# Performance work log

Measured on AMD Instinct MI355X. Metric: run time of the kernel, lower is better.

Reference implementation:

```python
import jax, jax.numpy as jnp
import numpy as np
from jax import lax

RHO = 1.0
L = 50

def _pbc_index(rho=RHO, L=L):
    # S = {(m,n) | |mn| <= rho*L//2, |m|<=L//2, |n|<=L//2}; rho*L//2 == 25.0 here
    thr = (rho * L) // 2
    idx = [(m, n)
           for m in range(-L // 2, L // 2 + 1)
           for n in range(-L // 2, L // 2 + 1)
           if abs(m * n) <= thr]
    return np.asarray(idx, dtype=np.int32)  # [T, 2], T = 449


def setup_inputs() -> dict:
    key = jax.random.key(0)
    k1, k2, k3, k4 = jax.random.split(key, 4)
    B, S, Nmodes = 8, 16384, 2
    T = _pbc_index().shape[0]  # 449
    return {
        "E_real": jax.random.normal(k1, (B, S, Nmodes), dtype=jnp.float32),
        "E_imag": jax.random.normal(k2, (B, S, Nmodes), dtype=jnp.float32),
        "C_real": jax.random.normal(k3, (4, T), dtype=jnp.float32) * 0.01,
        "C_imag": jax.random.normal(k4, (4, T), dtype=jnp.float32) * 0.01,
    }


def reference(E_real, E_imag, C_real, C_imag):
    idx = _pbc_index()
    m = jnp.asarray(idx[:, 0])
    n = jnp.asarray(idx[:, 1])
    E = E_real + 1j * E_imag                 # [B, S, 2] complex64
    C = (C_real + 1j * C_imag)[0]            # task_info=None -> row 0, [T]

    # O_k,i = E_k,i + sum_{m,n} (E_{k+n,i} E*_{k+m+n,i} + E_{k+n,-i} E*_{k+m+n,-i}) E_{k+m,i} C_{m,n}
    def body(acc, term):
        mi, ni, ci = term
        A = jnp.roll(E, ni, axis=-2) * jnp.conj(jnp.roll(E, mi + ni, axis=-2))
        A = A + jnp.roll(A, 1, axis=-1)      # cross-polarization term (Nmodes=2)
        return acc + A * jnp.roll(E, mi, axis=-2) * ci, None

    acc, _ = lax.scan(body, jnp.zeros_like(E), (m, n, C))
    Eo = E + acc                             # P = 1 (task_info=None), sqrt(P)**3 = 1
    return Eo[..., L:-L, :]                  # drop overlaps: [B, S-2L, 2]
```

## Files before the change

### kernel.cpp

```cpp
#include <hip/hip_runtime.h>


typedef float v2f __attribute__((ext_vector_type(2)));
typedef float v4f __attribute__((ext_vector_type(4)));

#define S_LEN 16384
#define SOUT  16284
#define BLK   512
#define NOUT  256
#define NE    356
#define NE2   178
#define ND    307
#define ND_AL 308
#define NDP   154

constexpr int LIMS[26] = {25,25,12,8,6,5,4,3,3,2,2,2,2,
                          1,1,1,1,1,1,1,1,1,1,1,1,1};
constexpr int TS[51] = {
      0,  3,  6,  9, 12, 15, 18, 21, 24, 27, 30, 33, 36,
     39, 44, 49, 54, 59, 66, 73, 82, 93,106,123,148,199,
    250,301,326,343,356,367,376,383,390,395,400,405,410,
    413,416,419,422,425,428,431,434,437,440,443,446};

template<int M>
__device__ __forceinline__ void convM(
    const float2* __restrict__ sDm, const v4f* __restrict__ sEp,
    int o0, const float* __restrict__ Cr0, const float* __restrict__ Ci0,
    float4& acc)
{
    constexpr int lim = LIMS[M];
    constexpr int tp  = TS[25 + M];
    constexpr int tn  = TS[25 - M];
    constexpr int A   = 25 + lim;

    v2f SxP0 = {0.f,0.f}, SyP0 = {0.f,0.f}, SxP1 = {0.f,0.f}, SyP1 = {0.f,0.f};
    v2f SxN0 = {0.f,0.f}, SyN0 = {0.f,0.f}, SxN1 = {0.f,0.f}, SyN1 = {0.f,0.f};

#define TAP(dconst, dd)                                                     \
    {                                                                       \
        const int d_ = (dconst);                                            \
        if (A - d_ >= 0 && A - d_ <= 2*lim) {                               \
            const float cx = Cr0[tp + A - d_], cy = Ci0[tp + A - d_];       \
            SxP0 += cx * (dd);  SyP0 += cy * (dd);                          \
        }                                                                   \
        if (A + 1 - d_ >= 0 && A + 1 - d_ <= 2*lim) {                       \
            const float cx = Cr0[tp + A+1-d_], cy = Ci0[tp + A+1-d_];       \
            SxP1 += cx * (dd);  SyP1 += cy * (dd);                          \
        }                                                                   \
        if (A + M - d_ >= 0 && A + M - d_ <= 2*lim) {                       \
            const float cx = Cr0[tn + A+M-d_], cy = Ci0[tn + A+M-d_];       \
            SxN0 += cx * (dd);  SyN0 += cy * (dd);                          \
        }                                                                   \
        if (A + M + 1 - d_ >= 0 && A + M + 1 - d_ <= 2*lim) {               \
            const float cx = Cr0[tn + A+M+1-d_], cy = Ci0[tn + A+M+1-d_];   \
            SxN1 += cx * (dd);  SyN1 += cy * (dd);                          \
        }                                                                   \
    }

    if constexpr (M < 2*lim + 4) {
        constexpr int dlo = (25 - lim) & ~1;
        constexpr int dhi = 26 + lim + M;
        constexpr int NP  = (dhi - dlo) / 2 + 1;
        #pragma unroll
        for (int p = 0; p < NP; ++p) {
            const int d0 = dlo + 2*p;
            v4f w = *reinterpret_cast<const v4f*>(&sDm[o0 + d0]);
            TAP(d0,     w.xy)
            TAP(d0 + 1, w.zw)
        }
    } else {
        {
            constexpr int dlo = (25 - lim) & ~1;
            constexpr int dhi = 26 + lim;
            constexpr int NP  = (dhi - dlo) / 2 + 1;
            #pragma unroll
            for (int p = 0; p < NP; ++p) {
                const int d0 = dlo + 2*p;
                v4f w = *reinterpret_cast<const v4f*>(&sDm[o0 + d0]);
                #pragma unroll
                for (int e = 0; e < 2; ++e) {
                    const int d = d0 + e;
                    const v2f dd = e ? w.zw : w.xy;
                    if (A - d >= 0 && A - d <= 2*lim) {
                        const float cx = Cr0[tp + A - d], cy = Ci0[tp + A - d];
                        SxP0 += cx * dd;  SyP0 += cy * dd;
                    }
                    if (A + 1 - d >= 0 && A + 1 - d <= 2*lim) {
                        const float cx = Cr0[tp + A+1-d], cy = Ci0[tp + A+1-d];
                        SxP1 += cx * dd;  SyP1 += cy * dd;
                    }
                }
            }
        }
        {
            constexpr int dlo = (25 + M - lim) & ~1;
            constexpr int dhi = 26 + M + lim;
            constexpr int NP  = (dhi - dlo) / 2 + 1;
            #pragma unroll
            for (int p = 0; p < NP; ++p) {
                const int d0 = dlo + 2*p;
                v4f w = *reinterpret_cast<const v4f*>(&sDm[o0 + d0]);
                #pragma unroll
                for (int e = 0; e < 2; ++e) {
                    const int d = d0 + e;
                    const v2f dd = e ? w.zw : w.xy;
                    if (A + M - d >= 0 && A + M - d <= 2*lim) {
                        const float cx = Cr0[tn + A+M-d], cy = Ci0[tn + A+M-d];
                        SxN0 += cx * dd;  SyN0 += cy * dd;
                    }
                    if (A + M + 1 - d >= 0 && A + M + 1 - d <= 2*lim) {
                        const float cx = Cr0[tn + A+M+1-d], cy = Ci0[tn + A+M+1-d];
                        SxN1 += cx * dd;  SyN1 += cy * dd;
                    }
                }
            }
        }
    }
#undef TAP

    const float s0pr = SxP0.x - SyP0.y, s0pi = SxP0.y + SyP0.x;
    const float s1pr = SxP1.x - SyP1.y, s1pi = SxP1.y + SyP1.x;
    const float s0nr = SxN0.x + SyN0.y, s0ni = SyN0.x - SxN0.y;
    const float s1nr = SxN1.x + SyN1.y, s1ni = SyN1.x - SxN1.y;

    const int t = o0 >> 1;
    v4f ep0, ep1, en0, en1;
    if constexpr ((M & 1) == 0) {
        ep0 = sEp[t + (50 - M)/2];
        ep1 = sEp[t + (50 - M)/2 + NE2];
        en0 = sEp[t + (50 + M)/2];
        en1 = sEp[t + (50 + M)/2 + NE2];
    } else {
        ep0 = sEp[t + (49 - M)/2 + NE2];
        ep1 = sEp[t + (51 - M)/2];
        en0 = sEp[t + (49 + M)/2 + NE2];
        en1 = sEp[t + (51 + M)/2];
    }
    acc.x += s0pr*ep0.x - s0pi*ep0.y + s0nr*en0.x - s0ni*en0.y;
    acc.y += s0pr*ep0.z - s0pi*ep0.w + s0nr*en0.z - s0ni*en0.w;
    acc.z += s1pr*ep1.x - s1pi*ep1.y + s1nr*en1.x - s1ni*en1.y;
    acc.w += s1pr*ep1.z - s1pi*ep1.w + s1nr*en1.z - s1ni*en1.w;
}

__device__ __forceinline__ void conv0(
    const float* __restrict__ sD0p, const v4f* __restrict__ sEp,
    int o0, const float* __restrict__ Cr0, const float* __restrict__ Ci0,
    float4& acc)
{
    v2f s0 = {0.f, 0.f}, s1 = {0.f, 0.f};
    #pragma unroll
    for (int p = 0; p < 26; ++p) {
        const int d0 = 2*p;
        float2 w = *reinterpret_cast<const float2*>(&sD0p[o0 + d0]);
        #pragma unroll
        for (int e = 0; e < 2; ++e) {
            const int d = d0 + e;
            const float dv = e ? w.y : w.x;
            if (50 - d >= 0) {
                v2f cv = { Cr0[199 + 50 - d], Ci0[199 + 50 - d] };
                s0 += dv * cv;
            }
            if (51 - d <= 50 && 51 - d >= 0) {
                v2f cv = { Cr0[199 + 51 - d], Ci0[199 + 51 - d] };
                s1 += dv * cv;
            }
        }
    }
    const int t = o0 >> 1;
    v4f e0 = sEp[t + 25];
    v4f e1 = sEp[t + 25 + NE2];
    acc.x += s0.x*e0.x - s0.y*e0.y;
    acc.y += s0.x*e0.z - s0.y*e0.w;
    acc.z += s1.x*e1.x - s1.y*e1.y;
    acc.w += s1.x*e1.z - s1.y*e1.w;
}

__global__ __launch_bounds__(BLK, 4) void pbc_kernel(
    const float* __restrict__ Er, const float* __restrict__ Ei,
    const float* __restrict__ Cr, const float* __restrict__ Ci,
    float* __restrict__ out)
{
    __shared__ __align__(16) v4f    sEp[NE];
    __shared__ __align__(16) float2 sD[25][ND_AL];
    __shared__ __align__(16) float  sD0[ND_AL];
    __shared__ __align__(16) float4 sAcc[4][128];

    const int b   = blockIdx.y;
    const int k0  = blockIdx.x * NOUT;
    const int tid = threadIdx.x;

    const float* erb = Er + (size_t)b * (S_LEN * 2);
    const float* eib = Ei + (size_t)b * (S_LEN * 2);
    if (tid < NE2) {
        const int i  = tid;
        const int kg = k0 + 2 * i;
        v4f rr = {0.f,0.f,0.f,0.f}, ii = {0.f,0.f,0.f,0.f};
        if (kg < S_LEN) {
            rr = *reinterpret_cast<const v4f*>(erb + 2 * kg);
            ii = *reinterpret_cast<const v4f*>(eib + 2 * kg);
        }
        sEp[i]       = (v4f){rr.x, ii.x, rr.y, ii.y};
        sEp[i + NE2] = (v4f){rr.z, ii.z, rr.w, ii.w};
    }
    __syncthreads();

    if (tid < NDP) {
        const int xp = tid;
        v4f a0 = sEp[xp + 12 + NE2];
        v4f a1 = sEp[xp + 13];
        float d0 = a0.x*a0.x + a0.y*a0.y + a0.z*a0.z + a0.w*a0.w;
        float d1 = a1.x*a1.x + a1.y*a1.y + a1.z*a1.z + a1.w*a1.w;
        *reinterpret_cast<float2*>(&sD0[2 * xp]) = make_float2(d0, d1);
    }
    for (int idx = tid; idx < 25 * NDP; idx += BLK) {
        const int m1 = idx / NDP;
        const int xp = idx - m1 * NDP;
        const int m  = m1 + 1;
        v4f a0 = sEp[xp + 12 + NE2];
        v4f a1 = sEp[xp + 13];
        const int sb  = 2 * xp + 25 - m;
        const int ib0 = (sb >> 1) + (sb & 1) * NE2;
        const int sb1 = sb + 1;
        const int ib1 = (sb1 >> 1) + (sb1 & 1) * NE2;
        v4f b0 = sEp[ib0], b1 = sEp[ib1];
        float gr0 = a0.x*b0.x + a0.y*b0.y + a0.z*b0.z + a0.w*b0.w;
        float gi0 = a0.y*b0.x - a0.x*b0.y + a0.w*b0.z - a0.z*b0.w;
        float gr1 = a1.x*b1.x + a1.y*b1.y + a1.z*b1.z + a1.w*b1.w;
        float gi1 = a1.y*b1.x - a1.x*b1.y + a1.w*b1.z - a1.z*b1.w;
        *reinterpret_cast<v4f*>(&sD[m1][2 * xp]) = (v4f){gr0, gi0, gr1, gi1};
    }
    __syncthreads();

    const int g  = tid >> 7;
    const int t  = tid & 127;
    const int o0 = 2 * t;

    float4 acc = make_float4(0.f, 0.f, 0.f, 0.f);
    if (g == 0) {
        convM<1>(sD[0],  sEp, o0, Cr, Ci, acc);
        convM<13>(sD[12], sEp, o0, Cr, Ci, acc);
    } else if (g == 1) {
        convM<2>(sD[1],  sEp, o0, Cr, Ci, acc);
        convM<3>(sD[2],  sEp, o0, Cr, Ci, acc);
        convM<6>(sD[5],  sEp, o0, Cr, Ci, acc);
        convM<14>(sD[13], sEp, o0, Cr, Ci, acc);
    } else if (g == 2) {
        conv0(sD0, sEp, o0, Cr, Ci, acc);
        convM<4>(sD[3],  sEp, o0, Cr, Ci, acc);
        convM<5>(sD[4],  sEp, o0, Cr, Ci, acc);
        convM<7>(sD[6],  sEp, o0, Cr, Ci, acc);
        convM<8>(sD[7],  sEp, o0, Cr, Ci, acc);
        convM<15>(sD[14], sEp, o0, Cr, Ci, acc);
    } else {
        convM<9>(sD[8],   sEp, o0, Cr, Ci, acc);
        convM<10>(sD[9],  sEp, o0, Cr, Ci, acc);
        convM<11>(sD[10], sEp, o0, Cr, Ci, acc);
        convM<12>(sD[11], sEp, o0, Cr, Ci, acc);
        convM<16>(sD[15], sEp, o0, Cr, Ci, acc);
        convM<17>(sD[16], sEp, o0, Cr, Ci, acc);
        convM<18>(sD[17], sEp, o0, Cr, Ci, acc);
        convM<19>(sD[18], sEp, o0, Cr, Ci, acc);
        convM<20>(sD[19], sEp, o0, Cr, Ci, acc);
        convM<21>(sD[20], sEp, o0, Cr, Ci, acc);
        convM<22>(sD[21], sEp, o0, Cr, Ci, acc);
        convM<23>(sD[22], sEp, o0, Cr, Ci, acc);
        convM<24>(sD[23], sEp, o0, Cr, Ci, acc);
        convM<25>(sD[24], sEp, o0, Cr, Ci, acc);
    }
    sAcc[g][t] = acc;
    __syncthreads();

    if (tid < 128) {
        const int tt = tid;
        const int oo = 2 * tt;
        const int ko = k0 + oo;
        if (ko < SOUT) {
            float4 p0 = sAcc[0][tt], p1 = sAcc[1][tt];
            float4 p2 = sAcc[2][tt], p3 = sAcc[3][tt];
            v4f e0 = sEp[tt + 25];
            v4f e1 = sEp[tt + 25 + NE2];
            float4 o;
            o.x = e0.x + p0.x + p1.x + p2.x + p3.x;
            o.y = e0.z + p0.y + p1.y + p2.y + p3.y;
            o.z = e1.x + p0.z + p1.z + p2.z + p3.z;
            o.w = e1.z + p0.w + p1.w + p2.w + p3.w;
            *reinterpret_cast<float4*>(out + ((size_t)b * SOUT + ko) * 2) = o;
        }
    }
}

extern "C" void kernel_launch(void* const* d_in, const int* in_sizes, int n_in,
                              void* d_out, int out_size, void* d_ws, size_t ws_size,
                              hipStream_t stream) {
    const float* Er = (const float*)d_in[0];
    const float* Ei = (const float*)d_in[1];
    const float* Cr = (const float*)d_in[2];
    const float* Ci = (const float*)d_in[3];
    float* out = (float*)d_out;

    dim3 grid((SOUT + NOUT - 1) / NOUT, 8);
    pbc_kernel<<<grid, BLK, 0, stream>>>(Er, Ei, Cr, Ci, out);
}
```

Before: 17.83 us.

## Stage coefficients in LDS as float2 and rebalance convolution work across wave groups

Copies the complex coefficient table into shared memory as interleaved float2, so each tap reads one LDS value instead of two separate global/scalar loads. Reassigns which M-diagonals each of the four thread groups handles, to even out per-group work. Group 0 now keeps its partial sum in registers and skips the sAcc write/read, which shrinks the shared reduction buffer. Moving the coefficients to LDS adds one shared table and more per-tap LDS traffic; the coefficient loads were uniform across threads and may previously have been served by scalar loads.

```diff
diff --git a/kernel.cpp b/kernel.cpp
--- a/kernel.cpp
+++ b/kernel.cpp
@@ -13,6 +13,7 @@
 #define ND    307
 #define ND_AL 308
 #define NDP   154
+#define T_CNT 449
 
 constexpr int LIMS[26] = {25,25,12,8,6,5,4,3,3,2,2,2,2,
                           1,1,1,1,1,1,1,1,1,1,1,1,1};
@@ -25,8 +26,7 @@
 template<int M>
 __device__ __forceinline__ void convM(
     const float2* __restrict__ sDm, const v4f* __restrict__ sEp,
-    int o0, const float* __restrict__ Cr0, const float* __restrict__ Ci0,
-    float4& acc)
+    const float2* __restrict__ sC, int o0, float4& acc)
 {
     constexpr int lim = LIMS[M];
     constexpr int tp  = TS[25 + M];
@@ -40,20 +40,20 @@
     {                                                                       \
         const int d_ = (dconst);                                            \
         if (A - d_ >= 0 && A - d_ <= 2*lim) {                               \
-            const float cx = Cr0[tp + A - d_], cy = Ci0[tp + A - d_];       \
-            SxP0 += cx * (dd);  SyP0 += cy * (dd);                          \
+            const float2 c = sC[tp + A - d_];                               \
+            SxP0 += c.x * (dd);  SyP0 += c.y * (dd);                        \
         }                                                                   \
         if (A + 1 - d_ >= 0 && A + 1 - d_ <= 2*lim) {                       \
-            const float cx = Cr0[tp + A+1-d_], cy = Ci0[tp + A+1-d_];       \
-            SxP1 += cx * (dd);  SyP1 += cy * (dd);                          \
+            const float2 c = sC[tp + A+1-d_];                               \
+            SxP1 += c.x * (dd);  SyP1 += c.y * (dd);                        \
         }                                                                   \
         if (A + M - d_ >= 0 && A + M - d_ <= 2*lim) {                       \
-            const float cx = Cr0[tn + A+M-d_], cy = Ci0[tn + A+M-d_];       \
-            SxN0 += cx * (dd);  SyN0 += cy * (dd);                          \
+            const float2 c = sC[tn + A+M-d_];                               \
+            SxN0 += c.x * (dd);  SyN0 += c.y * (dd);                        \
         }                                                                   \
         if (A + M + 1 - d_ >= 0 && A + M + 1 - d_ <= 2*lim) {               \
-            const float cx = Cr0[tn + A+M+1-d_], cy = Ci0[tn + A+M+1-d_];   \
-            SxN1 += cx * (dd);  SyN1 += cy * (dd);                          \
+            const float2 c = sC[tn + A+M+1-d_];                             \
+            SxN1 += c.x * (dd);  SyN1 += c.y * (dd);                        \
         }                                                                   \
     }
 
@@ -82,12 +82,12 @@
                     const int d = d0 + e;
                     const v2f dd = e ? w.zw : w.xy;
                     if (A - d >= 0 && A - d <= 2*lim) {
-                        const float cx = Cr0[tp + A - d], cy = Ci0[tp + A - d];
-                        SxP0 += cx * dd;  SyP0 += cy * dd;
+                        const float2 c = sC[tp + A - d];
+                        SxP0 += c.x * dd;  SyP0 += c.y * dd;
                     }
                     if (A + 1 - d >= 0 && A + 1 - d <= 2*lim) {
-                        const float cx = Cr0[tp + A+1-d], cy = Ci0[tp + A+1-d];
-                        SxP1 += cx * dd;  SyP1 += cy * dd;
+                        const float2 c = sC[tp + A+1-d];
+                        SxP1 += c.x * dd;  SyP1 += c.y * dd;
                     }
                 }
             }
@@ -105,12 +105,12 @@
                     const int d = d0 + e;
                     const v2f dd = e ? w.zw : w.xy;
                     if (A + M - d >= 0 && A + M - d <= 2*lim) {
-                        const float cx = Cr0[tn + A+M-d], cy = Ci0[tn + A+M-d];
-                        SxN0 += cx * dd;  SyN0 += cy * dd;
+                        const float2 c = sC[tn + A+M-d];
+                        SxN0 += c.x * dd;  SyN0 += c.y * dd;
                     }
                     if (A + M + 1 - d >= 0 && A + M + 1 - d <= 2*lim) {
-                        const float cx = Cr0[tn + A+M+1-d], cy = Ci0[tn + A+M+1-d];
-                        SxN1 += cx * dd;  SyN1 += cy * dd;
+                        const float2 c = sC[tn + A+M+1-d];
+                        SxN1 += c.x * dd;  SyN1 += c.y * dd;
                     }
                 }
             }
@@ -144,8 +144,7 @@
 
 __device__ __forceinline__ void conv0(
     const float* __restrict__ sD0p, const v4f* __restrict__ sEp,
-    int o0, const float* __restrict__ Cr0, const float* __restrict__ Ci0,
-    float4& acc)
+    const float2* __restrict__ sC, int o0, float4& acc)
 {
     v2f s0 = {0.f, 0.f}, s1 = {0.f, 0.f};
     #pragma unroll
@@ -157,12 +156,12 @@
             const int d = d0 + e;
             const float dv = e ? w.y : w.x;
             if (50 - d >= 0) {
-                v2f cv = { Cr0[199 + 50 - d], Ci0[199 + 50 - d] };
-                s0 += dv * cv;
+                const float2 c = sC[199 + 50 - d];
+                s0 += dv * (v2f){c.x, c.y};
             }
             if (51 - d <= 50 && 51 - d >= 0) {
-                v2f cv = { Cr0[199 + 51 - d], Ci0[199 + 51 - d] };
-                s1 += dv * cv;
+                const float2 c = sC[199 + 51 - d];
+                s1 += dv * (v2f){c.x, c.y};
             }
         }
     }
@@ -183,7 +182,8 @@
     __shared__ __align__(16) v4f    sEp[NE];
     __shared__ __align__(16) float2 sD[25][ND_AL];
     __shared__ __align__(16) float  sD0[ND_AL];
-    __shared__ __align__(16) float4 sAcc[4][128];
+    __shared__ __align__(16) float2 sC[T_CNT + 1];
+    __shared__ __align__(16) float4 sAcc[3][128];
 
     const int b   = blockIdx.y;
     const int k0  = blockIdx.x * NOUT;
@@ -202,6 +202,8 @@
         sEp[i]       = (v4f){rr.x, ii.x, rr.y, ii.y};
         sEp[i + NE2] = (v4f){rr.z, ii.z, rr.w, ii.w};
     }
+    for (int t = tid; t < T_CNT; t += BLK)
+        sC[t] = make_float2(Cr[t], Ci[t]);
     __syncthreads();
 
     if (tid < NDP) {
@@ -237,37 +239,37 @@
 
     float4 acc = make_float4(0.f, 0.f, 0.f, 0.f);
     if (g == 0) {
-        convM<1>(sD[0],  sEp, o0, Cr, Ci, acc);
-        convM<13>(sD[12], sEp, o0, Cr, Ci, acc);
+        convM<1>(sD[0],   sEp, sC, o0, acc);
+        convM<9>(sD[8],   sEp, sC, o0, acc);
+        convM<13>(sD[12], sEp, sC, o0, acc);
+        convM<14>(sD[13], sEp, sC, o0, acc);
+        convM<19>(sD[18], sEp, sC, o0, acc);
     } else if (g == 1) {
-        convM<2>(sD[1],  sEp, o0, Cr, Ci, acc);
-        convM<3>(sD[2],  sEp, o0, Cr, Ci, acc);
-        convM<6>(sD[5],  sEp, o0, Cr, Ci, acc);
-        convM<14>(sD[13], sEp, o0, Cr, Ci, acc);
+        convM<2>(sD[1],   sEp, sC, o0, acc);
+        convM<3>(sD[2],   sEp, sC, o0, acc);
+        convM<5>(sD[4],   sEp, sC, o0, acc);
+        convM<15>(sD[14], sEp, sC, o0, acc);
+        convM<16>(sD[15], sEp, sC, o0, acc);
+        convM<20>(sD[19], sEp, sC, o0, acc);
     } else if (g == 2) {
-        conv0(sD0, sEp, o0, Cr, Ci, acc);
-        convM<4>(sD[3],  sEp, o0, Cr, Ci, acc);
-        convM<5>(sD[4],  sEp, o0, Cr, Ci, acc);
-        convM<7>(sD[6],  sEp, o0, Cr, Ci, acc);
-        convM<8>(sD[7],  sEp, o0, Cr, Ci, acc);
-        convM<15>(sD[14], sEp, o0, Cr, Ci, acc);
+        conv0(sD0, sEp, sC, o0, acc);
+        convM<4>(sD[3],   sEp, sC, o0, acc);
+        convM<6>(sD[5],   sEp, sC, o0, acc);
+        convM<7>(sD[6],   sEp, sC, o0, acc);
+        convM<18>(sD[17], sEp, sC, o0, acc);
+        convM<21>(sD[20], sEp, sC, o0, acc);
     } else {
-        convM<9>(sD[8],   sEp, o0, Cr, Ci, acc);
-        convM<10>(sD[9],  sEp, o0, Cr, Ci, acc);
-        convM<11>(sD[10], sEp, o0, Cr, Ci, acc);
-        convM<12>(sD[11], sEp, o0, Cr, Ci, acc);
-        convM<16>(sD[15], sEp, o0, Cr, Ci, acc);
-        convM<17>(sD[16], sEp, o0, Cr, Ci, acc);
-        convM<18>(sD[17], sEp, o0, Cr, Ci, acc);
-        convM<19>(sD[18], sEp, o0, Cr, Ci, acc);
-        convM<20>(sD[19], sEp, o0, Cr, Ci, acc);
-        convM<21>(sD[20], sEp, o0, Cr, Ci, acc);
-        convM<22>(sD[21], sEp, o0, Cr, Ci, acc);
-        convM<23>(sD[22], sEp, o0, Cr, Ci, acc);
-        convM<24>(sD[23], sEp, o0, Cr, Ci, acc);
-        convM<25>(sD[24], sEp, o0, Cr, Ci, acc);
-    }
-    sAcc[g][t] = acc;
+        convM<8>(sD[7],   sEp, sC, o0, acc);
+        convM<10>(sD[9],  sEp, sC, o0, acc);
+        convM<11>(sD[10], sEp, sC, o0, acc);
+        convM<12>(sD[11], sEp, sC, o0, acc);
+        convM<17>(sD[16], sEp, sC, o0, acc);
+        convM<22>(sD[21], sEp, sC, o0, acc);
+        convM<23>(sD[22], sEp, sC, o0, acc);
+        convM<24>(sD[23], sEp, sC, o0, acc);
+        convM<25>(sD[24], sEp, sC, o0, acc);
+    }
+    if (g > 0) sAcc[g - 1][t] = acc;
     __syncthreads();
 
     if (tid < 128) {
@@ -275,15 +277,14 @@
         const int oo = 2 * tt;
         const int ko = k0 + oo;
         if (ko < SOUT) {
-            float4 p0 = sAcc[0][tt], p1 = sAcc[1][tt];
-            float4 p2 = sAcc[2][tt], p3 = sAcc[3][tt];
+            float4 p1 = sAcc[0][tt], p2 = sAcc[1][tt], p3 = sAcc[2][tt];
             v4f e0 = sEp[tt + 25];
             v4f e1 = sEp[tt + 25 + NE2];
             float4 o;
-            o.x = e0.x + p0.x + p1.x + p2.x + p3.x;
-            o.y = e0.z + p0.y + p1.y + p2.y + p3.y;
-            o.z = e1.x + p0.z + p1.z + p2.z + p3.z;
-            o.w = e1.z + p0.w + p1.w + p2.w + p3.w;
+            o.x = e0.x + acc.x + p1.x + p2.x + p3.x;
+            o.y = e0.z + acc.y + p1.y + p2.y + p3.y;
+            o.z = e1.x + acc.z + p1.z + p2.z + p3.z;
+            o.w = e1.z + acc.w + p1.w + p2.w + p3.w;
             *reinterpret_cast<float4*>(out + ((size_t)b * SOUT + ko) * 2) = o;
         }
     }
```

Measured after the change: 19.03 us. 1.07x slower.
